# Kernel optimization log

Hardware: AMD Instinct MI355X
Metric: run time of the kernel (lower is better)

Reference implementation:

```python
import jax, jax.numpy as jnp
import numpy as np

NHEAD = 8  # from init_kwargs
EPS = 1e-5  # nn.LayerNorm default


def _ln(x, w, b):
    mu = jnp.mean(x, axis=-1, keepdims=True)
    var = jnp.mean(jnp.square(x - mu), axis=-1, keepdims=True)
    return (x - mu) * jax.lax.rsqrt(var + EPS) * w + b


def setup_inputs() -> dict:
    key = jax.random.key(0)
    L, D, FF, B, S = 4, 256, 512, 2, 4096
    ks = jax.random.split(key, 14)
    s = 0.02
    inp = {
        "seq": jax.random.normal(ks[0], (B, S, D), jnp.float32),
        "Wqkv": jax.random.normal(ks[1], (L, 3 * D, D), jnp.float32) * s,
        "bqkv": jnp.zeros((L, 3 * D), jnp.float32),
        "Wo": jax.random.normal(ks[2], (L, D, D), jnp.float32) * s,
        "bo": jnp.zeros((L, D), jnp.float32),
        "ln1_w": jnp.ones((L, D), jnp.float32),
        "ln1_b": jnp.zeros((L, D), jnp.float32),
        "ln2_w": jnp.ones((L, D), jnp.float32),
        "ln2_b": jnp.zeros((L, D), jnp.float32),
        "W1": jax.random.normal(ks[3], (L, FF, D), jnp.float32) * s,
        "b1": jnp.zeros((L, FF), jnp.float32),
        "W2": jax.random.normal(ks[4], (L, D, FF), jnp.float32) * s,
        "b2": jnp.zeros((L, D), jnp.float32),
        "n_ctx": 2048,
    }
    return inp


def _forward(seq, Wqkv, bqkv, Wo, bo, ln1_w, ln1_b, ln2_w, ln2_b, W1, b1, W2, b2, n_ctx):
    B, S, D = seq.shape
    H = NHEAD
    hd = D // H
    scale = 1.0 / np.sqrt(hd).astype(np.float32)
    x = seq
    L = Wqkv.shape[0]
    for l in range(L):
        # pre-norm self-attention block (norm_first=True)
        h = _ln(x, ln1_w[l], ln1_b[l])
        qkv = h @ Wqkv[l].T + bqkv[l]            # [B,S,3D]
        q, k, v = jnp.split(qkv, 3, axis=-1)
        q = q.reshape(B, S, H, hd)
        # Mask structure: every token (context AND query) may only attend to
        # context keys [:n_ctx] -> keys/values restricted up-front, no dense
        # [S,S] score matrix and no explicit mask needed.
        kc = k[:, :n_ctx].reshape(B, n_ctx, H, hd)
        vc = v[:, :n_ctx].reshape(B, n_ctx, H, hd)
        scores = jnp.einsum('bqhd,bkhd->bhqk', q, kc) * scale  # [B,H,S,n_ctx]
        att = jax.nn.softmax(scores, axis=-1)
        o = jnp.einsum('bhqk,bkhd->bqhd', att, vc).reshape(B, S, D)
        x = x + o @ Wo[l].T + bo[l]
        # pre-norm feed-forward block, exact (erf) GELU as in PyTorch 'gelu'
        h2 = _ln(x, ln2_w[l], ln2_b[l])
        x = x + jax.nn.gelu(h2 @ W1[l].T + b1[l], approximate=False) @ W2[l].T + b2[l]
    return x


def reference(seq, Wqkv, bqkv, Wo, bo, ln1_w, ln1_b, ln2_w, ln2_b, W1, b1, W2, b2, n_ctx):
    return _forward(seq, Wqkv, bqkv, Wo, bo, ln1_w, ln1_b, ln2_w, ln2_b, W1, b1, W2, b2, n_ctx)
```

## Files before the change

### kernel.cpp

```cpp
#include <hip/hip_runtime.h>
#include <hip/hip_bf16.h>

#define BB 2
#define SS 4096
#define DD 256
#define FFD 512
#define NLAYER 4
#define NHEAD 8
#define HD 32
#define QKVD 768
#define NROWS 8192
#define NCTX 2048

typedef unsigned short u16;
typedef unsigned int   u32;
typedef __attribute__((ext_vector_type(8))) short short8;
typedef __attribute__((ext_vector_type(4))) short sv4;
typedef __attribute__((ext_vector_type(4))) float f32x4;

#if __has_builtin(__builtin_amdgcn_exp2f)
#define EXP2(x) __builtin_amdgcn_exp2f(x)
#else
#define EXP2(x) exp2f(x)
#endif

__device__ __forceinline__ float bf2f(u32 u) { return __uint_as_float(u << 16); }
__device__ __forceinline__ u16 f2bu(float f) {
    union { __hip_bfloat16 h; u16 u; } cv; cv.h = __float2bfloat16(f); return cv.u;
}
__device__ __forceinline__ float gelu_f(float v) {
    return 0.5f * v * (1.0f + erff(v * 0.70710678118654752f));
}

__global__ void copy_kernel(const float* __restrict__ in, float* __restrict__ out, int n) {
    int i = (blockIdx.x * blockDim.x + threadIdx.x) * 4;
    if (i >= n) return;
    *reinterpret_cast<float4*>(out + i) = *reinterpret_cast<const float4*>(in + i);
}

__global__ void f2bw4_kernel(const float* __restrict__ s0, const float* __restrict__ s1,
                             const float* __restrict__ s2, const float* __restrict__ s3,
                             u16* __restrict__ d0, u16* __restrict__ d1,
                             u16* __restrict__ d2, u16* __restrict__ d3) {
    int blk = blockIdx.x;
    const float* s; u16* d; int base;
    if (blk < 768)       { s = s0; d = d0; base = blk; }
    else if (blk < 1024) { s = s1; d = d1; base = blk - 768; }
    else if (blk < 1536) { s = s2; d = d2; base = blk - 1024; }
    else                 { s = s3; d = d3; base = blk - 1536; }
    int i = (base * 256 + threadIdx.x) * 4;
    float4 v = *reinterpret_cast<const float4*>(s + i);
    uint2 o;
    o.x = (u32)f2bu(v.x) | ((u32)f2bu(v.y) << 16);
    o.y = (u32)f2bu(v.z) | ((u32)f2bu(v.w) << 16);
    *reinterpret_cast<uint2*>(d + i) = o;
}

__global__ void ln_kernel(const float* __restrict__ x, const float* __restrict__ w,
                          const float* __restrict__ b, u16* __restrict__ out) {
    int row = blockIdx.x * 4 + (threadIdx.x >> 6);
    int lane = threadIdx.x & 63;
    int c = lane * 4;
    float4 v = *reinterpret_cast<const float4*>(x + (size_t)row * DD + c);
    float s  = v.x + v.y + v.z + v.w;
    float sq = v.x*v.x + v.y*v.y + v.z*v.z + v.w*v.w;
    #pragma unroll
    for (int off = 32; off >= 1; off >>= 1) {
        s  += __shfl_xor(s, off);
        sq += __shfl_xor(sq, off);
    }
    float mu   = s * (1.0f / DD);
    float var  = sq * (1.0f / DD) - mu * mu;
    float rstd = rsqrtf(var + 1e-5f);
    float4 wv = *reinterpret_cast<const float4*>(w + c);
    float4 bv = *reinterpret_cast<const float4*>(b + c);
    float o0 = (v.x - mu) * rstd * wv.x + bv.x;
    float o1 = (v.y - mu) * rstd * wv.y + bv.y;
    float o2 = (v.z - mu) * rstd * wv.z + bv.z;
    float o3 = (v.w - mu) * rstd * wv.w + bv.w;
    uint2 o;
    o.x = (u32)f2bu(o0) | ((u32)f2bu(o1) << 16);
    o.y = (u32)f2bu(o2) | ((u32)f2bu(o3) << 16);
    *reinterpret_cast<uint2*>(out + (size_t)row * DD + c) = o;
}

template<int TM, int ACT, int RES>
__global__ __launch_bounds__(256) void mfma_gemm(
        const u16* __restrict__ A, const u16* __restrict__ W, const float* __restrict__ bias,
        float* __restrict__ outf, u16* __restrict__ outb, int N, int K) {
    constexpr int MI = TM / 32;
    __shared__ __align__(16) u16 As[TM][136];
    __shared__ __align__(16) u16 Ws[64][136];
    int tid = threadIdx.x;
    int wave = tid >> 6, lane = tid & 63, la = lane & 15, quad = lane >> 4;
    int wm = (wave & 1) * (TM / 2), wn = (wave >> 1) * 32;
    int m0 = blockIdx.y * TM, n0 = blockIdx.x * 64;
    f32x4 acc[MI][2];
    #pragma unroll
    for (int mi = 0; mi < MI; mi++)
        #pragma unroll
        for (int ni = 0; ni < 2; ni++)
            acc[mi][ni] = (f32x4){0.f, 0.f, 0.f, 0.f};

    int ar = tid >> 4, ac = (tid & 15) * 8;
    for (int k0 = 0; k0 < K; k0 += 128) {
        #pragma unroll
        for (int p = 0; p < TM / 16; p++)
            *reinterpret_cast<uint4*>(&As[ar + p*16][ac]) =
                *reinterpret_cast<const uint4*>(&A[(size_t)(m0 + ar + p*16) * K + k0 + ac]);
        #pragma unroll
        for (int p = 0; p < 4; p++)
            *reinterpret_cast<uint4*>(&Ws[ar + p*16][ac]) =
                *reinterpret_cast<const uint4*>(&W[(size_t)(n0 + ar + p*16) * K + k0 + ac]);
        __syncthreads();
        #pragma unroll
        for (int kh = 0; kh < 4; kh++) {
            short8 af[MI], bf[2];
            #pragma unroll
            for (int mi = 0; mi < MI; mi++)
                af[mi] = *reinterpret_cast<const short8*>(&As[wm + mi*16 + la][kh*32 + quad*8]);
            #pragma unroll
            for (int ni = 0; ni < 2; ni++)
                bf[ni] = *reinterpret_cast<const short8*>(&Ws[wn + ni*16 + la][kh*32 + quad*8]);
            #pragma unroll
            for (int mi = 0; mi < MI; mi++)
                #pragma unroll
                for (int ni = 0; ni < 2; ni++)
                    acc[mi][ni] = __builtin_amdgcn_mfma_f32_16x16x32_bf16(af[mi], bf[ni], acc[mi][ni], 0, 0, 0);
        }
        __syncthreads();
    }

    #pragma unroll
    for (int mi = 0; mi < MI; mi++) {
        #pragma unroll
        for (int ni = 0; ni < 2; ni++) {
            int n = n0 + wn + ni*16 + la;
            float bv = bias[n];
            #pragma unroll
            for (int r = 0; r < 4; r++) {
                int m = m0 + wm + mi*16 + quad*4 + r;
                float v = acc[mi][ni][r] + bv;
                if (ACT) v = gelu_f(v);
                if (RES) outf[(size_t)m * N + n] += v;
                else     outb[(size_t)m * N + n] = f2bu(v);
            }
        }
    }
}

__global__ __launch_bounds__(256) void vtrans_kernel(const u16* __restrict__ qkv,
                                                     u16* __restrict__ vtg) {
    __shared__ __align__(16) u16 T[32][68];
    int tid = threadIdx.x;
    int kt = blockIdx.x, bh = blockIdx.y;
    int b = bh >> 3, hh = bh & 7;
    int key = tid >> 2, hd8 = (tid & 3) * 8;
    uint4 u = *reinterpret_cast<const uint4*>(
        &qkv[((size_t)b * SS + kt*64 + key) * QKVD + 2*DD + hh*32 + hd8]);
    int lowk = key & 31;
    int pos = (key & 32) | (((lowk >> 2) & 3) << 3) | (((lowk >> 4) & 1) << 2) | (lowk & 3);
    T[hd8 + 0][pos] = (u16)(u.x);  T[hd8 + 1][pos] = (u16)(u.x >> 16);
    T[hd8 + 2][pos] = (u16)(u.y);  T[hd8 + 3][pos] = (u16)(u.y >> 16);
    T[hd8 + 4][pos] = (u16)(u.z);  T[hd8 + 5][pos] = (u16)(u.z >> 16);
    T[hd8 + 6][pos] = (u16)(u.w);  T[hd8 + 7][pos] = (u16)(u.w >> 16);
    __syncthreads();
    int row = tid >> 3, cg = (tid & 7) * 8;
    sv4 lo = *reinterpret_cast<const sv4*>(&T[row][cg]);
    sv4 hi = *reinterpret_cast<const sv4*>(&T[row][cg + 4]);
    union { sv4 a[2]; uint4 u4; } cvt; cvt.a[0] = lo; cvt.a[1] = hi;
    *reinterpret_cast<uint4*>(&vtg[((size_t)bh*32 + row) * NCTX + kt*64 + cg]) = cvt.u4;
}

#define SCL2 0.2550437f
#define SH2  11.5415603f
__global__ __launch_bounds__(512, 4) void mfma_attn(const u16* __restrict__ qkv,
                                                    const u16* __restrict__ vtg,
                                                    u16* __restrict__ out) {
    __shared__ __align__(16) u16 smem[9728];
    u16 (*Ks)[64][40] = reinterpret_cast<u16(*)[64][40]>(smem);
    u16 (*Vt)[32][72] = reinterpret_cast<u16(*)[32][72]>(smem + 5120);

    int tid = threadIdx.x;
    int wv = tid >> 6, lane = tid & 63, la = lane & 15, quad = lane >> 4;
    int qw = wv & 3, ksp = wv >> 2;
    int bh = blockIdx.y, qidx = blockIdx.x;
    int b = bh >> 3, hh = bh & 7;
    size_t tokbase = (size_t)b * SS;
    int qb = qidx * 128 + qw * 32;

    short8 qf[2];
    #pragma unroll
    for (int qt = 0; qt < 2; qt++) {
        uint4 u = *reinterpret_cast<const uint4*>(
            &qkv[(tokbase + qb + qt*16 + la) * QKVD + hh*32 + quad*8]);
        union { short8 v; u16 e[8]; } qa;
        u32 w[4] = {u.x, u.y, u.z, u.w};
        #pragma unroll
        for (int i = 0; i < 4; i++) {
            qa.e[2*i]   = f2bu(bf2f(w[i] & 0xffffu) * SCL2);
            qa.e[2*i+1] = f2bu(bf2f(w[i] >> 16) * SCL2);
        }
        qf[qt] = qa.v;
    }

    f32x4 o[2][2];
    #pragma unroll
    for (int i = 0; i < 2; i++)
        #pragma unroll
        for (int j = 0; j < 2; j++) o[i][j] = (f32x4){0.f, 0.f, 0.f, 0.f};
    f32x4 l_acc[2];
    l_acc[0] = (f32x4){0.f, 0.f, 0.f, 0.f};
    l_acc[1] = (f32x4){0.f, 0.f, 0.f, 0.f};
    const f32x4 cinit = (f32x4){-SH2, -SH2, -SH2, -SH2};
    short8 onesf;
    { union { short8 v; u16 e[8]; } t;
      #pragma unroll
      for (int i = 0; i < 8; i++) t.e[i] = 0x3F80;
      onesf = t.v; }

    int sr = tid >> 2, sk = (tid & 3) * 8;
    int hs = sr >> 6, krow = sr & 63;
    int vr = tid >> 4, vc = (tid & 15) * 8;
    int vh = vc >> 6, vcol = vc & 63;
    const u16* kgp = &qkv[(tokbase + hs*1024 + krow) * QKVD + DD + hh*32 + sk];
    const u16* vgp = &vtg[((size_t)bh*32 + vr) * NCTX + vh*1024 + vcol];
    uint4 kreg = *reinterpret_cast<const uint4*>(kgp);
    uint4 vreg = *reinterpret_cast<const uint4*>(vgp);

    for (int step = 0; step < 16; step++) {
        *reinterpret_cast<uint4*>(&Ks[hs][krow][sk]) = kreg;
        *reinterpret_cast<uint4*>(&Vt[vh][vr][vcol]) = vreg;
        __syncthreads();
        if (step < 15) {
            kreg = *reinterpret_cast<const uint4*>(kgp + (size_t)(step+1)*64*QKVD);
            vreg = *reinterpret_cast<const uint4*>(vgp + (step+1)*64);
        }

        #pragma unroll
        for (int c = 0; c < 2; c++) {
            short8 kf0 = *reinterpret_cast<const short8*>(&Ks[ksp][c*32 + la][quad*8]);
            short8 kf1 = *reinterpret_cast<const short8*>(&Ks[ksp][c*32 + 16 + la][quad*8]);
            f32x4 s00 = __builtin_amdgcn_mfma_f32_16x16x32_bf16(kf0, qf[0], cinit, 0, 0, 0);
            f32x4 s10 = __builtin_amdgcn_mfma_f32_16x16x32_bf16(kf1, qf[0], cinit, 0, 0, 0);
            f32x4 s01 = __builtin_amdgcn_mfma_f32_16x16x32_bf16(kf0, qf[1], cinit, 0, 0, 0);
            f32x4 s11 = __builtin_amdgcn_mfma_f32_16x16x32_bf16(kf1, qf[1], cinit, 0, 0, 0);

            union { uint4 u; short8 v; } pf0, pf1;
            {
                u32 a0 = __float_as_uint(EXP2(s00[0])), a1 = __float_as_uint(EXP2(s00[1]));
                u32 a2 = __float_as_uint(EXP2(s00[2])), a3 = __float_as_uint(EXP2(s00[3]));
                u32 b0 = __float_as_uint(EXP2(s10[0])), b1 = __float_as_uint(EXP2(s10[1]));
                u32 b2 = __float_as_uint(EXP2(s10[2])), b3 = __float_as_uint(EXP2(s10[3]));
                pf0.u.x = __builtin_amdgcn_perm(a1, a0, 0x07060302u);
                pf0.u.y = __builtin_amdgcn_perm(a3, a2, 0x07060302u);
                pf0.u.z = __builtin_amdgcn_perm(b1, b0, 0x07060302u);
                pf0.u.w = __builtin_amdgcn_perm(b3, b2, 0x07060302u);
            }
            {
                u32 a0 = __float_as_uint(EXP2(s01[0])), a1 = __float_as_uint(EXP2(s01[1]));
                u32 a2 = __float_as_uint(EXP2(s01[2])), a3 = __float_as_uint(EXP2(s01[3]));
                u32 b0 = __float_as_uint(EXP2(s11[0])), b1 = __float_as_uint(EXP2(s11[1]));
                u32 b2 = __float_as_uint(EXP2(s11[2])), b3 = __float_as_uint(EXP2(s11[3]));
                pf1.u.x = __builtin_amdgcn_perm(a1, a0, 0x07060302u);
                pf1.u.y = __builtin_amdgcn_perm(a3, a2, 0x07060302u);
                pf1.u.z = __builtin_amdgcn_perm(b1, b0, 0x07060302u);
                pf1.u.w = __builtin_amdgcn_perm(b3, b2, 0x07060302u);
            }

            l_acc[0] = __builtin_amdgcn_mfma_f32_16x16x32_bf16(onesf, pf0.v, l_acc[0], 0, 0, 0);
            l_acc[1] = __builtin_amdgcn_mfma_f32_16x16x32_bf16(onesf, pf1.v, l_acc[1], 0, 0, 0);

            short8 vf0 = *reinterpret_cast<const short8*>(&Vt[ksp][la][c*32 + quad*8]);
            short8 vf1 = *reinterpret_cast<const short8*>(&Vt[ksp][16 + la][c*32 + quad*8]);
            o[0][0] = __builtin_amdgcn_mfma_f32_16x16x32_bf16(vf0, pf0.v, o[0][0], 0, 0, 0);
            o[0][1] = __builtin_amdgcn_mfma_f32_16x16x32_bf16(vf0, pf1.v, o[0][1], 0, 0, 0);
            o[1][0] = __builtin_amdgcn_mfma_f32_16x16x32_bf16(vf1, pf0.v, o[1][0], 0, 0, 0);
            o[1][1] = __builtin_amdgcn_mfma_f32_16x16x32_bf16(vf1, pf1.v, o[1][1], 0, 0, 0);
        }
        __syncthreads();
    }

    float* obuf = reinterpret_cast<float*>(smem);
    if (wv >= 4) {
        int idx = (qw * 64 + lane) * 18;
        #pragma unroll
        for (int mio = 0; mio < 2; mio++)
            #pragma unroll
            for (int qt = 0; qt < 2; qt++)
                #pragma unroll
                for (int r = 0; r < 4; r++)
                    obuf[idx + mio*8 + qt*4 + r] = o[mio][qt][r];
        obuf[idx + 16] = l_acc[0][0];
        obuf[idx + 17] = l_acc[1][0];
    }
    __syncthreads();
    if (wv < 4) {
        int idx = (qw * 64 + lane) * 18;
        #pragma unroll
        for (int mio = 0; mio < 2; mio++)
            #pragma unroll
            for (int qt = 0; qt < 2; qt++)
                #pragma unroll
                for (int r = 0; r < 4; r++)
                    o[mio][qt][r] += obuf[idx + mio*8 + qt*4 + r];
        float liq[2];
        liq[0] = 1.0f / (l_acc[0][0] + obuf[idx + 16]);
        liq[1] = 1.0f / (l_acc[1][0] + obuf[idx + 17]);
        #pragma unroll
        for (int qt = 0; qt < 2; qt++) {
            float li = liq[qt];
            size_t token = tokbase + qb + qt*16 + la;
            #pragma unroll
            for (int mio = 0; mio < 2; mio++) {
                uint2 w;
                w.x = (u32)f2bu(o[mio][qt][0] * li) | ((u32)f2bu(o[mio][qt][1] * li) << 16);
                w.y = (u32)f2bu(o[mio][qt][2] * li) | ((u32)f2bu(o[mio][qt][3] * li) << 16);
                *reinterpret_cast<uint2*>(&out[token * DD + hh*32 + mio*16 + quad*4]) = w;
            }
        }
    }
}

extern "C" void kernel_launch(void* const* d_in, const int* in_sizes, int n_in,
                              void* d_out, int out_size, void* d_ws, size_t ws_size,
                              hipStream_t stream) {
    const float* seq   = (const float*)d_in[0];
    const float* Wqkv  = (const float*)d_in[1];
    const float* bqkv  = (const float*)d_in[2];
    const float* Wo    = (const float*)d_in[3];
    const float* bo    = (const float*)d_in[4];
    const float* ln1w  = (const float*)d_in[5];
    const float* ln1b  = (const float*)d_in[6];
    const float* ln2w  = (const float*)d_in[7];
    const float* ln2b  = (const float*)d_in[8];
    const float* W1    = (const float*)d_in[9];
    const float* b1    = (const float*)d_in[10];
    const float* W2    = (const float*)d_in[11];
    const float* b2    = (const float*)d_in[12];

    const int NX = NROWS * DD;
    float* x    = (float*)d_out;
    char* wsb   = (char*)d_ws;
    u16*  qkv   = (u16*)wsb;
    u16*  ff    = qkv;
    u16*  h     = (u16*)(wsb + 12582912);
    u16*  hln   = (u16*)(wsb + 16777216);
    u16*  wbf   = (u16*)(wsb + 20971520);
    u16*  vtg   = (u16*)(wsb + 25165824);
    u16* wqkv_b = wbf;
    u16* wo_b   = wbf + 786432;
    u16* w1_b   = wbf + 1048576;
    u16* w2_b   = wbf + 1572864;

    f2bw4_kernel<<<2048, 256, 0, stream>>>(Wqkv, Wo, W1, W2, wqkv_b, wo_b, w1_b, w2_b);
    copy_kernel<<<NX/1024, 256, 0, stream>>>(seq, x, NX);

    for (int l = 0; l < NLAYER; l++) {
        ln_kernel<<<NROWS/4, 256, 0, stream>>>(x, ln1w + l*DD, ln1b + l*DD, hln);
        mfma_gemm<128,0,0><<<dim3(QKVD/64, NROWS/128), 256, 0, stream>>>(
            hln, wqkv_b + (size_t)l*QKVD*DD, bqkv + l*QKVD, nullptr, qkv, QKVD, DD);
        vtrans_kernel<<<dim3(NCTX/64, BB*NHEAD), 256, 0, stream>>>(qkv, vtg);
        mfma_attn<<<dim3(SS/128, BB*NHEAD), 512, 0, stream>>>(qkv, vtg, h);
        mfma_gemm<64,0,1><<<dim3(DD/64, NROWS/64), 256, 0, stream>>>(
            h, wo_b + (size_t)l*DD*DD, bo + l*DD, x, nullptr, DD, DD);
        ln_kernel<<<NROWS/4, 256, 0, stream>>>(x, ln2w + l*DD, ln2b + l*DD, hln);
        mfma_gemm<128,1,0><<<dim3(FFD/64, NROWS/128), 256, 0, stream>>>(
            hln, w1_b + (size_t)l*FFD*DD, b1 + l*FFD, nullptr, ff, FFD, DD);
        mfma_gemm<64,0,1><<<dim3(DD/64, NROWS/64), 256, 0, stream>>>(
            ff, w2_b + (size_t)l*DD*FFD, b2 + l*DD, x, nullptr, DD, FFD);
    }
}
```

Before: 401.9 us.

## Fuse residual GEMMs with following LayerNorm and merge init kernels

Replaces the Wo and W2 residual GEMMs with a full-row kernel in which each 512-thread block owns 32 complete rows of 256 columns. The kernel adds bias and the residual, then computes the next LayerNorm in the epilogue, so the separate ln_kernel launches and their extra pass over x disappear. The weight conversion, the seq copy and the first LayerNorm are merged into a single init kernel. The new GEMM reads A and W straight from global memory without LDS tiling, which may cost extra load bandwidth. It also launches only 256 blocks, giving lower parallelism.

Measured after the change: 440.3 us. 1.1x slower.

```diff
diff --git a/kernel.cpp b/kernel.cpp
--- a/kernel.cpp
+++ b/kernel.cpp
@@ -32,62 +32,60 @@
     return 0.5f * v * (1.0f + erff(v * 0.70710678118654752f));
 }
 
-__global__ void copy_kernel(const float* __restrict__ in, float* __restrict__ out, int n) {
-    int i = (blockIdx.x * blockDim.x + threadIdx.x) * 4;
-    if (i >= n) return;
-    *reinterpret_cast<float4*>(out + i) = *reinterpret_cast<const float4*>(in + i);
-}
-
-__global__ void f2bw4_kernel(const float* __restrict__ s0, const float* __restrict__ s1,
-                             const float* __restrict__ s2, const float* __restrict__ s3,
-                             u16* __restrict__ d0, u16* __restrict__ d1,
-                             u16* __restrict__ d2, u16* __restrict__ d3) {
+__global__ __launch_bounds__(256) void init_kernel(
+        const float* __restrict__ s0, const float* __restrict__ s1,
+        const float* __restrict__ s2, const float* __restrict__ s3,
+        u16* __restrict__ d0, u16* __restrict__ d1,
+        u16* __restrict__ d2, u16* __restrict__ d3,
+        const float* __restrict__ seq, float* __restrict__ x,
+        const float* __restrict__ lw, const float* __restrict__ lb,
+        u16* __restrict__ hln) {
     int blk = blockIdx.x;
-    const float* s; u16* d; int base;
-    if (blk < 768)       { s = s0; d = d0; base = blk; }
-    else if (blk < 1024) { s = s1; d = d1; base = blk - 768; }
-    else if (blk < 1536) { s = s2; d = d2; base = blk - 1024; }
-    else                 { s = s3; d = d3; base = blk - 1536; }
-    int i = (base * 256 + threadIdx.x) * 4;
-    float4 v = *reinterpret_cast<const float4*>(s + i);
-    uint2 o;
-    o.x = (u32)f2bu(v.x) | ((u32)f2bu(v.y) << 16);
-    o.y = (u32)f2bu(v.z) | ((u32)f2bu(v.w) << 16);
-    *reinterpret_cast<uint2*>(d + i) = o;
-}
-
-__global__ void ln_kernel(const float* __restrict__ x, const float* __restrict__ w,
-                          const float* __restrict__ b, u16* __restrict__ out) {
-    int row = blockIdx.x * 4 + (threadIdx.x >> 6);
-    int lane = threadIdx.x & 63;
-    int c = lane * 4;
-    float4 v = *reinterpret_cast<const float4*>(x + (size_t)row * DD + c);
-    float s  = v.x + v.y + v.z + v.w;
-    float sq = v.x*v.x + v.y*v.y + v.z*v.z + v.w*v.w;
-    #pragma unroll
-    for (int off = 32; off >= 1; off >>= 1) {
-        s  += __shfl_xor(s, off);
-        sq += __shfl_xor(sq, off);
-    }
-    float mu   = s * (1.0f / DD);
-    float var  = sq * (1.0f / DD) - mu * mu;
-    float rstd = rsqrtf(var + 1e-5f);
-    float4 wv = *reinterpret_cast<const float4*>(w + c);
-    float4 bv = *reinterpret_cast<const float4*>(b + c);
-    float o0 = (v.x - mu) * rstd * wv.x + bv.x;
-    float o1 = (v.y - mu) * rstd * wv.y + bv.y;
-    float o2 = (v.z - mu) * rstd * wv.z + bv.z;
-    float o3 = (v.w - mu) * rstd * wv.w + bv.w;
-    uint2 o;
-    o.x = (u32)f2bu(o0) | ((u32)f2bu(o1) << 16);
-    o.y = (u32)f2bu(o2) | ((u32)f2bu(o3) << 16);
-    *reinterpret_cast<uint2*>(out + (size_t)row * DD + c) = o;
-}
-
-template<int TM, int ACT, int RES>
+    if (blk < 2048) {
+        const float* s; u16* d; int base;
+        if (blk < 768)       { s = s0; d = d0; base = blk; }
+        else if (blk < 1024) { s = s1; d = d1; base = blk - 768; }
+        else if (blk < 1536) { s = s2; d = d2; base = blk - 1024; }
+        else                 { s = s3; d = d3; base = blk - 1536; }
+        int i = (base * 256 + threadIdx.x) * 4;
+        float4 v = *reinterpret_cast<const float4*>(s + i);
+        uint2 o;
+        o.x = (u32)f2bu(v.x) | ((u32)f2bu(v.y) << 16);
+        o.y = (u32)f2bu(v.z) | ((u32)f2bu(v.w) << 16);
+        *reinterpret_cast<uint2*>(d + i) = o;
+    } else {
+        int row = (blk - 2048) * 4 + (threadIdx.x >> 6);
+        int lane = threadIdx.x & 63;
+        int c = lane * 4;
+        float4 v = *reinterpret_cast<const float4*>(seq + (size_t)row * DD + c);
+        *reinterpret_cast<float4*>(x + (size_t)row * DD + c) = v;
+        float s  = v.x + v.y + v.z + v.w;
+        float sq = v.x*v.x + v.y*v.y + v.z*v.z + v.w*v.w;
+        #pragma unroll
+        for (int off = 32; off >= 1; off >>= 1) {
+            s  += __shfl_xor(s, off);
+            sq += __shfl_xor(sq, off);
+        }
+        float mu   = s * (1.0f / DD);
+        float var  = sq * (1.0f / DD) - mu * mu;
+        float rstd = rsqrtf(var + 1e-5f);
+        float4 wv = *reinterpret_cast<const float4*>(lw + c);
+        float4 bv = *reinterpret_cast<const float4*>(lb + c);
+        float o0 = (v.x - mu) * rstd * wv.x + bv.x;
+        float o1 = (v.y - mu) * rstd * wv.y + bv.y;
+        float o2 = (v.z - mu) * rstd * wv.z + bv.z;
+        float o3 = (v.w - mu) * rstd * wv.w + bv.w;
+        uint2 o;
+        o.x = (u32)f2bu(o0) | ((u32)f2bu(o1) << 16);
+        o.y = (u32)f2bu(o2) | ((u32)f2bu(o3) << 16);
+        *reinterpret_cast<uint2*>(hln + (size_t)row * DD + c) = o;
+    }
+}
+
+template<int TM, int ACT>
 __global__ __launch_bounds__(256) void mfma_gemm(
         const u16* __restrict__ A, const u16* __restrict__ W, const float* __restrict__ bias,
-        float* __restrict__ outf, u16* __restrict__ outb, int N, int K) {
+        u16* __restrict__ outb, int N, int K) {
     constexpr int MI = TM / 32;
     __shared__ __align__(16) u16 As[TM][136];
     __shared__ __align__(16) u16 Ws[64][136];
@@ -142,9 +140,106 @@
                 int m = m0 + wm + mi*16 + quad*4 + r;
                 float v = acc[mi][ni][r] + bv;
                 if (ACT) v = gelu_f(v);
-                if (RES) outf[(size_t)m * N + n] += v;
-                else     outb[(size_t)m * N + n] = f2bu(v);
-            }
+                outb[(size_t)m * N + n] = f2bu(v);
+            }
+        }
+    }
+}
+
+template<int K, int WLN>
+__global__ __launch_bounds__(512) void gemm_res_ln(
+        const u16* __restrict__ A, const u16* __restrict__ W, const float* __restrict__ bias,
+        const float* __restrict__ lw, const float* __restrict__ lb,
+        float* __restrict__ x, u16* __restrict__ hln) {
+    __shared__ float red[4][32][2];
+    int tid = threadIdx.x;
+    int wv = tid >> 6, lane = tid & 63, la = lane & 15, quad = lane >> 4;
+    int wrow = (wv >> 2) * 16, wn = (wv & 3) * 64;
+    int m0 = blockIdx.x * 32;
+    int mrb = m0 + wrow + quad * 4;
+
+    float xv[4][4], bv[4], lwv[4], lbv[4];
+    #pragma unroll
+    for (int ni = 0; ni < 4; ni++) {
+        int n = wn + ni*16 + la;
+        bv[ni] = bias[n];
+        if (WLN) { lwv[ni] = lw[n]; lbv[ni] = lb[n]; }
+        #pragma unroll
+        for (int r = 0; r < 4; r++)
+            xv[ni][r] = x[(size_t)(mrb + r) * DD + n];
+    }
+
+    f32x4 acc[4];
+    #pragma unroll
+    for (int ni = 0; ni < 4; ni++) acc[ni] = (f32x4){0.f, 0.f, 0.f, 0.f};
+
+    const u16* Ap = &A[(size_t)(m0 + wrow + la) * K];
+    #pragma unroll
+    for (int kh = 0; kh < K / 32; kh++) {
+        short8 af = *reinterpret_cast<const short8*>(&Ap[kh*32 + quad*8]);
+        #pragma unroll
+        for (int ni = 0; ni < 4; ni++) {
+            short8 bf = *reinterpret_cast<const short8*>(
+                &W[(size_t)(wn + ni*16 + la) * K + kh*32 + quad*8]);
+            acc[ni] = __builtin_amdgcn_mfma_f32_16x16x32_bf16(af, bf, acc[ni], 0, 0, 0);
+        }
+    }
+
+    float t[4][4], s[4], sq[4];
+    #pragma unroll
+    for (int r = 0; r < 4; r++) { s[r] = 0.f; sq[r] = 0.f; }
+    #pragma unroll
+    for (int ni = 0; ni < 4; ni++)
+        #pragma unroll
+        for (int r = 0; r < 4; r++) {
+            float v = acc[ni][r] + bv[ni] + xv[ni][r];
+            t[ni][r] = v;
+            s[r] += v; sq[r] += v * v;
+        }
+
+    if (WLN) {
+        #pragma unroll
+        for (int off = 1; off <= 8; off <<= 1)
+            #pragma unroll
+            for (int r = 0; r < 4; r++) {
+                s[r]  += __shfl_xor(s[r],  off);
+                sq[r] += __shfl_xor(sq[r], off);
+            }
+        if (la == 0) {
+            #pragma unroll
+            for (int r = 0; r < 4; r++) {
+                red[wv & 3][wrow + quad*4 + r][0] = s[r];
+                red[wv & 3][wrow + quad*4 + r][1] = sq[r];
+            }
+        }
+        __syncthreads();
+        float mu[4], rs[4];
+        #pragma unroll
+        for (int r = 0; r < 4; r++) {
+            int row = wrow + quad*4 + r;
+            float S = red[0][row][0] + red[1][row][0] + red[2][row][0] + red[3][row][0];
+            float Q = red[0][row][1] + red[1][row][1] + red[2][row][1] + red[3][row][1];
+            mu[r] = S * (1.0f / DD);
+            float var = Q * (1.0f / DD) - mu[r] * mu[r];
+            rs[r] = rsqrtf(var + 1e-5f);
+        }
+        #pragma unroll
+        for (int ni = 0; ni < 4; ni++) {
+            int n = wn + ni*16 + la;
+            #pragma unroll
+            for (int r = 0; r < 4; r++) {
+                x[(size_t)(mrb + r) * DD + n] = t[ni][r];
+                hln[(size_t)(mrb + r) * DD + n] =
+                    f2bu((t[ni][r] - mu[r]) * rs[r] * lwv[ni] + lbv[ni]);
+            }
+        }
+    } else {
+        #pragma unroll
+        for (int ni = 0; ni < 4; ni++) {
+            int n = wn + ni*16 + la;
+            #pragma unroll
+            for (int r = 0; r < 4; r++)
+                x[(size_t)(mrb + r) * DD + n] = t[ni][r];
         }
     }
 }
@@ -339,7 +434,6 @@
     const float* W2    = (const float*)d_in[11];
     const float* b2    = (const float*)d_in[12];
 
-    const int NX = NROWS * DD;
     float* x    = (float*)d_out;
     char* wsb   = (char*)d_ws;
     u16*  qkv   = (u16*)wsb;
@@ -353,21 +447,24 @@
     u16* w1_b   = wbf + 1048576;
     u16* w2_b   = wbf + 1572864;
 
-    f2bw4_kernel<<<2048, 256, 0, stream>>>(Wqkv, Wo, W1, W2, wqkv_b, wo_b, w1_b, w2_b);
-    copy_kernel<<<NX/1024, 256, 0, stream>>>(seq, x, NX);
+    init_kernel<<<4096, 256, 0, stream>>>(Wqkv, Wo, W1, W2, wqkv_b, wo_b, w1_b, w2_b,
+                                          seq, x, ln1w, ln1b, hln);
 
     for (int l = 0; l < NLAYER; l++) {
-        ln_kernel<<<NROWS/4, 256, 0, stream>>>(x, ln1w + l*DD, ln1b + l*DD, hln);
-        mfma_gemm<128,0,0><<<dim3(QKVD/64, NROWS/128), 256, 0, stream>>>(
-            hln, wqkv_b + (size_t)l*QKVD*DD, bqkv + l*QKVD, nullptr, qkv, QKVD, DD);
+        mfma_gemm<128,0><<<dim3(QKVD/64, NROWS/128), 256, 0, stream>>>(
+            hln, wqkv_b + (size_t)l*QKVD*DD, bqkv + l*QKVD, qkv, QKVD, DD);
         vtrans_kernel<<<dim3(NCTX/64, BB*NHEAD), 256, 0, stream>>>(qkv, vtg);
         mfma_attn<<<dim3(SS/128, BB*NHEAD), 512, 0, stream>>>(qkv, vtg, h);
-        mfma_gemm<64,0,1><<<dim3(DD/64, NROWS/64), 256, 0, stream>>>(
-            h, wo_b + (size_t)l*DD*DD, bo + l*DD, x, nullptr, DD, DD);
-        ln_kernel<<<NROWS/4, 256, 0, stream>>>(x, ln2w + l*DD, ln2b + l*DD, hln);
-        mfma_gemm<128,1,0><<<dim3(FFD/64, NROWS/128), 256, 0, stream>>>(
-            hln, w1_b + (size_t)l*FFD*DD, b1 + l*FFD, nullptr, ff, FFD, DD);
-        mfma_gemm<64,0,1><<<dim3(DD/64, NROWS/64), 256, 0, stream>>>(
-            ff, w2_b + (size_t)l*DD*FFD, b2 + l*DD, x, nullptr, DD, FFD);
-    }
-}
+        gemm_res_ln<256,1><<<NROWS/32, 512, 0, stream>>>(
+            h, wo_b + (size_t)l*DD*DD, bo + l*DD, ln2w + l*DD, ln2b + l*DD, x, hln);
+        mfma_gemm<128,1><<<dim3(FFD/64, NROWS/128), 256, 0, stream>>>(
+            hln, w1_b + (size_t)l*FFD*DD, b1 + l*FFD, ff, FFD, DD);
+        if (l < NLAYER - 1)
+            gemm_res_ln<512,1><<<NROWS/32, 512, 0, stream>>>(
+                ff, w2_b + (size_t)l*DD*FFD, b2 + l*DD,
+                ln1w + (l+1)*DD, ln1b + (l+1)*DD, x, hln);
+        else
+            gemm_res_ln<512,0><<<NROWS/32, 512, 0, stream>>>(
+                ff, w2_b + (size_t)l*DD*FFD, b2 + l*DD, nullptr, nullptr, x, nullptr);
+    }
+}
```

## Fuse V-transpose into QKV GEMM epilogue and merge init kernels

Applied to the files above, without the earlier changes.

The QKV GEMM now writes the transposed V block for context rows straight into the vtg buffer from its accumulators, which removes the separate vtrans kernel launch and its re-read of qkv. The weight conversion, the seq-to-x copy and the first-layer LayerNorm are merged into one init kernel, and each later layer's ln1 is launched at the end of the previous iteration. Together these cut launch count and some memory traffic. In exchange the QKV GEMM epilogue does extra strided 8-byte stores into vtg that depend on a specific key-ordering permutation.

Measured after the change: 390.3 us. 2.9% less time.

```diff
diff --git a/kernel.cpp b/kernel.cpp
--- a/kernel.cpp
+++ b/kernel.cpp
@@ -32,28 +32,54 @@
     return 0.5f * v * (1.0f + erff(v * 0.70710678118654752f));
 }
 
-__global__ void copy_kernel(const float* __restrict__ in, float* __restrict__ out, int n) {
-    int i = (blockIdx.x * blockDim.x + threadIdx.x) * 4;
-    if (i >= n) return;
-    *reinterpret_cast<float4*>(out + i) = *reinterpret_cast<const float4*>(in + i);
-}
-
-__global__ void f2bw4_kernel(const float* __restrict__ s0, const float* __restrict__ s1,
-                             const float* __restrict__ s2, const float* __restrict__ s3,
-                             u16* __restrict__ d0, u16* __restrict__ d1,
-                             u16* __restrict__ d2, u16* __restrict__ d3) {
+__global__ __launch_bounds__(256) void init_kernel(
+        const float* __restrict__ s0, const float* __restrict__ s1,
+        const float* __restrict__ s2, const float* __restrict__ s3,
+        u16* __restrict__ d0, u16* __restrict__ d1,
+        u16* __restrict__ d2, u16* __restrict__ d3,
+        const float* __restrict__ seq, float* __restrict__ x,
+        const float* __restrict__ lw, const float* __restrict__ lb,
+        u16* __restrict__ hln) {
     int blk = blockIdx.x;
-    const float* s; u16* d; int base;
-    if (blk < 768)       { s = s0; d = d0; base = blk; }
-    else if (blk < 1024) { s = s1; d = d1; base = blk - 768; }
-    else if (blk < 1536) { s = s2; d = d2; base = blk - 1024; }
-    else                 { s = s3; d = d3; base = blk - 1536; }
-    int i = (base * 256 + threadIdx.x) * 4;
-    float4 v = *reinterpret_cast<const float4*>(s + i);
-    uint2 o;
-    o.x = (u32)f2bu(v.x) | ((u32)f2bu(v.y) << 16);
-    o.y = (u32)f2bu(v.z) | ((u32)f2bu(v.w) << 16);
-    *reinterpret_cast<uint2*>(d + i) = o;
+    if (blk < 2048) {
+        const float* s; u16* d; int base;
+        if (blk < 768)       { s = s0; d = d0; base = blk; }
+        else if (blk < 1024) { s = s1; d = d1; base = blk - 768; }
+        else if (blk < 1536) { s = s2; d = d2; base = blk - 1024; }
+        else                 { s = s3; d = d3; base = blk - 1536; }
+        int i = (base * 256 + threadIdx.x) * 4;
+        float4 v = *reinterpret_cast<const float4*>(s + i);
+        uint2 o;
+        o.x = (u32)f2bu(v.x) | ((u32)f2bu(v.y) << 16);
+        o.y = (u32)f2bu(v.z) | ((u32)f2bu(v.w) << 16);
+        *reinterpret_cast<uint2*>(d + i) = o;
+    } else {
+        int row = (blk - 2048) * 4 + (threadIdx.x >> 6);
+        int lane = threadIdx.x & 63;
+        int c = lane * 4;
+        float4 v = *reinterpret_cast<const float4*>(seq + (size_t)row * DD + c);
+        *reinterpret_cast<float4*>(x + (size_t)row * DD + c) = v;
+        float s  = v.x + v.y + v.z + v.w;
+        float sq = v.x*v.x + v.y*v.y + v.z*v.z + v.w*v.w;
+        #pragma unroll
+        for (int off = 32; off >= 1; off >>= 1) {
+            s  += __shfl_xor(s, off);
+            sq += __shfl_xor(sq, off);
+        }
+        float mu   = s * (1.0f / DD);
+        float var  = sq * (1.0f / DD) - mu * mu;
+        float rstd = rsqrtf(var + 1e-5f);
+        float4 wv = *reinterpret_cast<const float4*>(lw + c);
+        float4 bv = *reinterpret_cast<const float4*>(lb + c);
+        float o0 = (v.x - mu) * rstd * wv.x + bv.x;
+        float o1 = (v.y - mu) * rstd * wv.y + bv.y;
+        float o2 = (v.z - mu) * rstd * wv.z + bv.z;
+        float o3 = (v.w - mu) * rstd * wv.w + bv.w;
+        uint2 o;
+        o.x = (u32)f2bu(o0) | ((u32)f2bu(o1) << 16);
+        o.y = (u32)f2bu(o2) | ((u32)f2bu(o3) << 16);
+        *reinterpret_cast<uint2*>(hln + (size_t)row * DD + c) = o;
+    }
 }
 
 __global__ void ln_kernel(const float* __restrict__ x, const float* __restrict__ w,
@@ -84,10 +110,11 @@
     *reinterpret_cast<uint2*>(out + (size_t)row * DD + c) = o;
 }
 
-template<int TM, int ACT, int RES>
+template<int TM, int ACT, int RES, int WV>
 __global__ __launch_bounds__(256) void mfma_gemm(
         const u16* __restrict__ A, const u16* __restrict__ W, const float* __restrict__ bias,
-        float* __restrict__ outf, u16* __restrict__ outb, int N, int K) {
+        float* __restrict__ outf, u16* __restrict__ outb, u16* __restrict__ vtg,
+        int N, int K) {
     constexpr int MI = TM / 32;
     __shared__ __align__(16) u16 As[TM][136];
     __shared__ __align__(16) u16 Ws[64][136];
@@ -147,29 +174,28 @@
             }
         }
     }
-}
-
-__global__ __launch_bounds__(256) void vtrans_kernel(const u16* __restrict__ qkv,
-                                                     u16* __restrict__ vtg) {
-    __shared__ __align__(16) u16 T[32][68];
-    int tid = threadIdx.x;
-    int kt = blockIdx.x, bh = blockIdx.y;
-    int b = bh >> 3, hh = bh & 7;
-    int key = tid >> 2, hd8 = (tid & 3) * 8;
-    uint4 u = *reinterpret_cast<const uint4*>(
-        &qkv[((size_t)b * SS + kt*64 + key) * QKVD + 2*DD + hh*32 + hd8]);
-    int lowk = key & 31;
-    int pos = (key & 32) | (((lowk >> 2) & 3) << 3) | (((lowk >> 4) & 1) << 2) | (lowk & 3);
-    T[hd8 + 0][pos] = (u16)(u.x);  T[hd8 + 1][pos] = (u16)(u.x >> 16);
-    T[hd8 + 2][pos] = (u16)(u.y);  T[hd8 + 3][pos] = (u16)(u.y >> 16);
-    T[hd8 + 4][pos] = (u16)(u.z);  T[hd8 + 5][pos] = (u16)(u.z >> 16);
-    T[hd8 + 6][pos] = (u16)(u.w);  T[hd8 + 7][pos] = (u16)(u.w >> 16);
-    __syncthreads();
-    int row = tid >> 3, cg = (tid & 7) * 8;
-    sv4 lo = *reinterpret_cast<const sv4*>(&T[row][cg]);
-    sv4 hi = *reinterpret_cast<const sv4*>(&T[row][cg + 4]);
-    union { sv4 a[2]; uint4 u4; } cvt; cvt.a[0] = lo; cvt.a[1] = hi;
-    *reinterpret_cast<uint4*>(&vtg[((size_t)bh*32 + row) * NCTX + kt*64 + cg]) = cvt.u4;
+
+    if (WV) {
+        if ((n0 >= 2*DD) && ((m0 & (SS-1)) < NCTX)) {
+            int b = m0 >> 12;
+            int kb = ((m0 + wm) & (SS-1)) + quad*8;
+            #pragma unroll
+            for (int mi = 0; mi < MI; mi++) {
+                int chunk = kb + (mi >> 1)*32 + (mi & 1)*4;
+                #pragma unroll
+                for (int ni = 0; ni < 2; ni++) {
+                    int n = n0 + wn + ni*16 + la;
+                    int vc = n - 2*DD;
+                    float bv = bias[n];
+                    u16* dst = &vtg[((size_t)((b << 3) + (vc >> 5)) * 32 + (vc & 31)) * NCTX + chunk];
+                    uint2 w;
+                    w.x = (u32)f2bu(acc[mi][ni][0] + bv) | ((u32)f2bu(acc[mi][ni][1] + bv) << 16);
+                    w.y = (u32)f2bu(acc[mi][ni][2] + bv) | ((u32)f2bu(acc[mi][ni][3] + bv) << 16);
+                    *reinterpret_cast<uint2*>(dst) = w;
+                }
+            }
+        }
+    }
 }
 
 #define SCL2 0.2550437f
@@ -339,7 +365,6 @@
     const float* W2    = (const float*)d_in[11];
     const float* b2    = (const float*)d_in[12];
 
-    const int NX = NROWS * DD;
     float* x    = (float*)d_out;
     char* wsb   = (char*)d_ws;
     u16*  qkv   = (u16*)wsb;
@@ -353,21 +378,21 @@
     u16* w1_b   = wbf + 1048576;
     u16* w2_b   = wbf + 1572864;
 
-    f2bw4_kernel<<<2048, 256, 0, stream>>>(Wqkv, Wo, W1, W2, wqkv_b, wo_b, w1_b, w2_b);
-    copy_kernel<<<NX/1024, 256, 0, stream>>>(seq, x, NX);
+    init_kernel<<<4096, 256, 0, stream>>>(Wqkv, Wo, W1, W2, wqkv_b, wo_b, w1_b, w2_b,
+                                          seq, x, ln1w, ln1b, hln);
 
     for (int l = 0; l < NLAYER; l++) {
-        ln_kernel<<<NROWS/4, 256, 0, stream>>>(x, ln1w + l*DD, ln1b + l*DD, hln);
-        mfma_gemm<128,0,0><<<dim3(QKVD/64, NROWS/128), 256, 0, stream>>>(
-            hln, wqkv_b + (size_t)l*QKVD*DD, bqkv + l*QKVD, nullptr, qkv, QKVD, DD);
-        vtrans_kernel<<<dim3(NCTX/64, BB*NHEAD), 256, 0, stream>>>(qkv, vtg);
+        mfma_gemm<128,0,0,1><<<dim3(QKVD/64, NROWS/128), 256, 0, stream>>>(
+            hln, wqkv_b + (size_t)l*QKVD*DD, bqkv + l*QKVD, nullptr, qkv, vtg, QKVD, DD);
         mfma_attn<<<dim3(SS/128, BB*NHEAD), 512, 0, stream>>>(qkv, vtg, h);
-        mfma_gemm<64,0,1><<<dim3(DD/64, NROWS/64), 256, 0, stream>>>(
-            h, wo_b + (size_t)l*DD*DD, bo + l*DD, x, nullptr, DD, DD);
+        mfma_gemm<64,0,1,0><<<dim3(DD/64, NROWS/64), 256, 0, stream>>>(
+            h, wo_b + (size_t)l*DD*DD, bo + l*DD, x, nullptr, nullptr, DD, DD);
         ln_kernel<<<NROWS/4, 256, 0, stream>>>(x, ln2w + l*DD, ln2b + l*DD, hln);
-        mfma_gemm<128,1,0><<<dim3(FFD/64, NROWS/128), 256, 0, stream>>>(
-            hln, w1_b + (size_t)l*FFD*DD, b1 + l*FFD, nullptr, ff, FFD, DD);
-        mfma_gemm<64,0,1><<<dim3(DD/64, NROWS/64), 256, 0, stream>>>(
-            ff, w2_b + (size_t)l*DD*FFD, b2 + l*DD, x, nullptr, DD, FFD);
-    }
-}
+        mfma_gemm<128,1,0,0><<<dim3(FFD/64, NROWS/128), 256, 0, stream>>>(
+            hln, w1_b + (size_t)l*FFD*DD, b1 + l*FFD, nullptr, ff, nullptr, FFD, DD);
+        mfma_gemm<64,0,1,0><<<dim3(DD/64, NROWS/64), 256, 0, stream>>>(
+            ff, w2_b + (size_t)l*DD*FFD, b2 + l*DD, x, nullptr, nullptr, DD, FFD);
+        if (l < NLAYER - 1)
+            ln_kernel<<<NROWS/4, 256, 0, stream>>>(x, ln1w + (l+1)*DD, ln1b + (l+1)*DD, hln);
+    }
+}
```
